# Optimization experiments

Hardware: AMD Instinct MI355X
Metric: run time of the kernel (lower is better)

Reference implementation:

```python
import jax, jax.numpy as jnp
import numpy as np

N = 4096
STD = 0.01


def setup_inputs() -> dict:
    key = jax.random.key(0)
    ks = jax.random.split(key, 16)
    p = lambda k, shape: STD * jax.random.normal(k, shape, dtype=jnp.float32)
    return {
        "t": 0,
        "x": jax.random.normal(ks[0], (N, 1), dtype=jnp.float32),
        "A": jax.random.normal(ks[1], (N, N), dtype=jnp.float32),
        # MLP_A: 2 -> 16 -> 16 -> 1 (ReLU between hidden layers), torch (out,in) layout
        "WA0": p(ks[2], (16, 2)), "bA0": p(ks[3], (16,)),
        "WA1": p(ks[4], (16, 16)), "bA1": p(ks[5], (16,)),
        "WA2": p(ks[6], (1, 16)), "bA2": p(ks[7], (1,)),
        # MLP: 1 -> 16 -> 1 (ReLU after first layer)
        "Wm0": p(ks[8], (16, 1)), "bm0": p(ks[9], (16,)),
        "Wm1": p(ks[10], (1, 16)), "bm1": p(ks[11], (1,)),
        # linear_A: 2 -> 1, no bias; linear_f: 1 -> 1, no bias
        "wA": p(ks[12], (1, 2)),
        "wf": p(ks[13], (1, 1)),
    }


def reference(t, x, A, WA0, bA0, WA1, bA1, WA2, bA2, Wm0, bm0, Wm1, bm1, wA, wf):
    n = x.shape[0]
    # node MLP branch: hidden_list[0] == 1 != 0
    x_N = jax.nn.relu(x @ Wm0.T + bm0) @ Wm1.T + bm1 + x @ wf.T  # (n, 1)
    # all-pairs features: x_a[i, j] = (x_i, x_j)
    x1 = jnp.broadcast_to(x, (n, n))       # row i = x_i repeated
    x2 = jnp.broadcast_to(x.T, (n, n))     # row i = full x vector
    x_a = jnp.stack((x1, x2), axis=-1)     # (n, n, 2)
    # edge MLP (2 -> 16 -> 16 -> 1) + skip linear_A (2 -> 1)
    h = jax.nn.relu(x_a @ WA0.T + bA0)     # (n, n, 16)
    h = jax.nn.relu(h @ WA1.T + bA1)       # (n, n, 16)
    x_e = (h @ WA2.T + bA2)[..., 0]        # (n, n)
    x_12 = (x_a @ wA.T)[..., 0]            # (n, n)
    # adjacency-weighted reduction over neighbors (dim=1)
    x_A = jnp.sum(A * (x_e + x_12), axis=1, keepdims=True)  # (n, 1)
    return x_N + x_A
```

## Files before the change

### kernel.cpp

```cpp
#include <hip/hip_runtime.h>
#include <hip/hip_bf16.h>


#define NN 4096

typedef __fp16 half8  __attribute__((ext_vector_type(8)));
typedef __fp16 half2v __attribute__((ext_vector_type(2)));
typedef __attribute__((ext_vector_type(4)))  float f32x4;
typedef __attribute__((ext_vector_type(16))) float f32x16;

__device__ __forceinline__ half2v cvt2(float lo, float hi) {
    return __builtin_amdgcn_cvt_pkrtz(lo, hi);
}

__global__ __launch_bounds__(256, 4) void odef_kernel(
    const float* __restrict__ x,  const float* __restrict__ A,
    const float* __restrict__ WA0, const float* __restrict__ bA0,
    const float* __restrict__ WA1, const float* __restrict__ bA1,
    const float* __restrict__ WA2, const float* __restrict__ bA2,
    const float* __restrict__ Wm0, const float* __restrict__ bm0,
    const float* __restrict__ Wm1, const float* __restrict__ bm1,
    const float* __restrict__ wA,  const float* __restrict__ wf,
    float* __restrict__ out)
{
    __shared__ float xs[NN];

    const int tid  = threadIdx.x;
    const int wave = tid >> 6;
    const int lane = tid & 63;
    const int n    = lane & 31;
    const int half = lane >> 5;
    const int row  = blockIdx.x * 4 + wave;

    {
        const f32x4* xsrc = (const f32x4*)x;
        f32x4* xdst = (f32x4*)xs;
        #pragma unroll
        for (int i = 0; i < 4; ++i)
            xdst[tid + 256 * i] = xsrc[tid + 256 * i];
    }
    const float xi = x[row];

    union { half2v h2[4]; half8 h8; } au;
    #pragma unroll
    for (int p = 0; p < 4; ++p) {
        float lo = 0.f, hi = 0.f;
        if (n < 16) {
            int k = half * 8 + p * 2;
            lo = WA1[n * 16 + k];
            hi = WA1[n * 16 + k + 1];
        }
        au.h2[p] = cvt2(lo, hi);
    }

    half2v u2h[4], w2h[4];
    #pragma unroll
    for (int p = 0; p < 4; ++p) {
        int k0 = half * 8 + p * 2;
        u2h[p] = cvt2(fmaf(WA0[2 * k0],     xi, bA0[k0]),
                      fmaf(WA0[2 * k0 + 2], xi, bA0[k0 + 1]));
        w2h[p] = cvt2(WA0[2 * k0 + 1], WA0[2 * k0 + 3]);
    }

    half2v wa2h[4], bb[4];
    #pragma unroll
    for (int p = 0; p < 4; ++p) {
        int r  = 2 * p;
        int m0 = (r & 3) + 8 * (r >> 2) + 4 * half;
        wa2h[p] = cvt2(WA2[m0], WA2[m0 + 1]);
        bb[p]   = cvt2(bA1[m0], bA1[m0 + 1]);
    }

    const float wA1h = half ? 0.f : wA[1];
    const float c0h  = half ? 0.f : (bA2[0] + wA[0] * xi);
    const half2v z2 = { (__fp16)0.f, (__fp16)0.f };
    const f32x16 zc = {};

    float acc0 = 0.f, acc1 = 0.f;

    auto body = [&](const f32x4 xv, const f32x4 av) {
        #pragma unroll
        for (int q = 0; q < 4; q += 2) {
            half2v xg0 = cvt2(xv[q], xv[q]);
            union { half2v h2[4]; half8 h8; } b0;
            #pragma unroll
            for (int p = 0; p < 4; ++p)
                b0.h2[p] = __builtin_elementwise_max(w2h[p] * xg0 + u2h[p], z2);
            f32x16 d0 = __builtin_amdgcn_mfma_f32_32x32x16_f16(au.h8, b0.h8, zc, 0, 0, 0);

            half2v xg1 = cvt2(xv[q + 1], xv[q + 1]);
            union { half2v h2[4]; half8 h8; } b1;
            #pragma unroll
            for (int p = 0; p < 4; ++p)
                b1.h2[p] = __builtin_elementwise_max(w2h[p] * xg1 + u2h[p], z2);
            f32x16 d1 = __builtin_amdgcn_mfma_f32_32x32x16_f16(au.h8, b1.h8, zc, 0, 0, 0);

            {
                float pp = fmaf(wA1h, xv[q], c0h);
                #pragma unroll
                for (int p = 0; p < 4; ++p) {
                    half2v t = __builtin_elementwise_max(
                        cvt2(d0[2 * p], d0[2 * p + 1]) + bb[p], z2);
                    pp = __builtin_amdgcn_fdot2(t, wa2h[p], pp, false);
                }
                acc0 = fmaf(av[q], pp, acc0);
            }
            {
                float pp = fmaf(wA1h, xv[q + 1], c0h);
                #pragma unroll
                for (int p = 0; p < 4; ++p) {
                    half2v t = __builtin_elementwise_max(
                        cvt2(d1[2 * p], d1[2 * p + 1]) + bb[p], z2);
                    pp = __builtin_amdgcn_fdot2(t, wa2h[p], pp, false);
                }
                acc1 = fmaf(av[q + 1], pp, acc1);
            }
        }
    };

    __syncthreads();

    const float* ap = A + (size_t)row * NN + 4 * n;
    const f32x4* xls = (const f32x4*)xs;

#define LOADA(dst, p) \
    asm volatile("global_load_dwordx4 %0, %1, off" : "=v"(dst) : "v"(p))
#define WAITV(N) do {                                              \
    asm volatile("s_waitcnt vmcnt(" #N ")" ::: "memory");          \
    __builtin_amdgcn_sched_barrier(0); } while (0)

    __builtin_amdgcn_sched_barrier(0);
    asm volatile("s_waitcnt vmcnt(0)" ::: "memory");
    __builtin_amdgcn_sched_barrier(0);

    f32x4 L0,  L1,  L2,  L3,  L4,  L5,  L6,  L7,
          L8,  L9,  L10, L11, L12, L13, L14, L15,
          L16, L17, L18, L19, L20, L21, L22, L23,
          L24, L25, L26, L27, L28, L29, L30, L31;

    LOADA(L0, ap + 128 * 0);  LOADA(L1, ap + 128 * 1);
    LOADA(L2, ap + 128 * 2);  LOADA(L3, ap + 128 * 3);
    LOADA(L4, ap + 128 * 4);  LOADA(L5, ap + 128 * 5);
    LOADA(L6, ap + 128 * 6);  LOADA(L7, ap + 128 * 7);

#define STEPM(T, CUR, NXT) {                                       \
        f32x4 xv = xls[n + 32 * (T)];                              \
        WAITV(7);                                                  \
        body(xv, CUR);                                             \
        LOADA(NXT, ap + 128 * ((T) + 8)); }

    STEPM(0,  L0,  L8)   STEPM(1,  L1,  L9)   STEPM(2,  L2,  L10)
    STEPM(3,  L3,  L11)  STEPM(4,  L4,  L12)  STEPM(5,  L5,  L13)
    STEPM(6,  L6,  L14)  STEPM(7,  L7,  L15)  STEPM(8,  L8,  L16)
    STEPM(9,  L9,  L17)  STEPM(10, L10, L18)  STEPM(11, L11, L19)
    STEPM(12, L12, L20)  STEPM(13, L13, L21)  STEPM(14, L14, L22)
    STEPM(15, L15, L23)  STEPM(16, L16, L24)  STEPM(17, L17, L25)
    STEPM(18, L18, L26)  STEPM(19, L19, L27)  STEPM(20, L20, L28)
    STEPM(21, L21, L29)  STEPM(22, L22, L30)  STEPM(23, L23, L31)

#define STEPT(T, WN, CUR) {                                        \
        f32x4 xv = xls[n + 32 * (T)];                              \
        WAITV(WN);                                                 \
        body(xv, CUR); }

    STEPT(24, 7, L24) STEPT(25, 6, L25) STEPT(26, 5, L26) STEPT(27, 4, L27)
    STEPT(28, 3, L28) STEPT(29, 2, L29) STEPT(30, 1, L30) STEPT(31, 0, L31)

#undef STEPM
#undef STEPT
#undef LOADA
#undef WAITV

    float acc = acc0 + acc1;
    #pragma unroll
    for (int off = 32; off > 0; off >>= 1)
        acc += __shfl_xor(acc, off);

    if (lane == 0) {
        float xn = fmaf(wf[0], xi, bm1[0]);
        #pragma unroll
        for (int h = 0; h < 16; ++h)
            xn = fmaf(Wm1[h], fmaxf(fmaf(Wm0[h], xi, bm0[h]), 0.f), xn);
        out[row] = xn + acc;
    }
}

extern "C" void kernel_launch(void* const* d_in, const int* in_sizes, int n_in,
                              void* d_out, int out_size, void* d_ws, size_t ws_size,
                              hipStream_t stream) {
    const float* x   = (const float*)d_in[1];
    const float* A   = (const float*)d_in[2];
    const float* WA0 = (const float*)d_in[3];
    const float* bA0 = (const float*)d_in[4];
    const float* WA1 = (const float*)d_in[5];
    const float* bA1 = (const float*)d_in[6];
    const float* WA2 = (const float*)d_in[7];
    const float* bA2 = (const float*)d_in[8];
    const float* Wm0 = (const float*)d_in[9];
    const float* bm0 = (const float*)d_in[10];
    const float* Wm1 = (const float*)d_in[11];
    const float* bm1 = (const float*)d_in[12];
    const float* wA  = (const float*)d_in[13];
    const float* wf  = (const float*)d_in[14];
    float* out = (float*)d_out;

    odef_kernel<<<NN / 4, 256, 0, stream>>>(x, A, WA0, bA0, WA1, bA1, WA2, bA2,
                                            Wm0, bm0, Wm1, bm1, wA, wf, out);
}
```

Before: 145.3 us.

## Pre-convert A to interleaved fp16 in workspace before the main reduction kernel

Adds a conversion kernel that casts A from fp32 to fp16 into the workspace, in an interleaved layout so that each 16-byte load brings eight A values for a lane. The main kernel then streams half the bytes for A and converts them back to fp32 before the same MFMA edge-MLP body. The conversion kernel runs on every call, so it adds a full fp32 read plus an fp16 write of A on top of the main kernel's fp16 read. It also lowers the precision of A. The old fp32 kernel is kept as a fallback when the workspace is too small.

```diff
diff --git a/kernel.cpp b/kernel.cpp
--- a/kernel.cpp
+++ b/kernel.cpp
@@ -13,8 +13,30 @@
     return __builtin_amdgcn_cvt_pkrtz(lo, hi);
 }
 
-__global__ __launch_bounds__(256, 4) void odef_kernel(
-    const float* __restrict__ x,  const float* __restrict__ A,
+__global__ __launch_bounds__(256, 8) void conv_kernel(
+    const float* __restrict__ A, __fp16* __restrict__ B)
+{
+    const int nitems = NN * NN / 8;
+    const int stride = gridDim.x * blockDim.x;
+    for (int i = blockIdx.x * blockDim.x + threadIdx.x; i < nitems; i += stride) {
+        const int row = i >> 9;
+        const int rem = i & 511;
+        const int P = rem >> 5;
+        const int n = rem & 31;
+        const float* s = A + (size_t)row * NN + P * 256 + n * 4;
+        f32x4 lo = *(const f32x4*)s;
+        f32x4 hi = *(const f32x4*)(s + 128);
+        half8 h;
+        h[0] = (__fp16)lo[0]; h[1] = (__fp16)lo[1];
+        h[2] = (__fp16)lo[2]; h[3] = (__fp16)lo[3];
+        h[4] = (__fp16)hi[0]; h[5] = (__fp16)hi[1];
+        h[6] = (__fp16)hi[2]; h[7] = (__fp16)hi[3];
+        *(half8*)(B + (size_t)i * 8) = h;
+    }
+}
+
+__global__ __launch_bounds__(256, 4) void odef_f16(
+    const __fp16* __restrict__ A16, const float* __restrict__ x,
     const float* __restrict__ WA0, const float* __restrict__ bA0,
     const float* __restrict__ WA1, const float* __restrict__ bA1,
     const float* __restrict__ WA2, const float* __restrict__ bA2,
@@ -120,6 +142,182 @@
 
     __syncthreads();
 
+    const __fp16* ap = A16 + (size_t)row * NN + 8 * n;
+    const f32x4* xls = (const f32x4*)xs;
+
+#define LOADA(dst, p) \
+    asm volatile("global_load_dwordx4 %0, %1, off" : "=v"(dst) : "v"(p))
+#define WAITV(N) do {                                              \
+    asm volatile("s_waitcnt vmcnt(" #N ")" ::: "memory");          \
+    __builtin_amdgcn_sched_barrier(0); } while (0)
+
+    __builtin_amdgcn_sched_barrier(0);
+    asm volatile("s_waitcnt vmcnt(0)" ::: "memory");
+    __builtin_amdgcn_sched_barrier(0);
+
+    half8 L0, L1, L2,  L3,  L4,  L5,  L6,  L7,
+          L8, L9, L10, L11, L12, L13, L14, L15;
+
+    LOADA(L0, ap + 256 * 0);  LOADA(L1, ap + 256 * 1);
+    LOADA(L2, ap + 256 * 2);  LOADA(L3, ap + 256 * 3);
+    LOADA(L4, ap + 256 * 4);  LOADA(L5, ap + 256 * 5);
+    LOADA(L6, ap + 256 * 6);  LOADA(L7, ap + 256 * 7);
+
+#define STEPM(T, CUR, NXT) {                                       \
+        f32x4 xa = xls[n + 64 * (T)];                              \
+        f32x4 xb = xls[n + 64 * (T) + 32];                         \
+        WAITV(7);                                                  \
+        f32x4 avA = { (float)CUR[0], (float)CUR[1],                \
+                      (float)CUR[2], (float)CUR[3] };              \
+        f32x4 avB = { (float)CUR[4], (float)CUR[5],                \
+                      (float)CUR[6], (float)CUR[7] };              \
+        body(xa, avA);                                             \
+        body(xb, avB);                                             \
+        LOADA(NXT, ap + 256 * ((T) + 8)); }
+
+    STEPM(0, L0, L8)  STEPM(1, L1, L9)  STEPM(2, L2, L10) STEPM(3, L3, L11)
+    STEPM(4, L4, L12) STEPM(5, L5, L13) STEPM(6, L6, L14) STEPM(7, L7, L15)
+
+#define STEPT(T, WN, CUR) {                                        \
+        f32x4 xa = xls[n + 64 * (T)];                              \
+        f32x4 xb = xls[n + 64 * (T) + 32];                         \
+        WAITV(WN);                                                 \
+        f32x4 avA = { (float)CUR[0], (float)CUR[1],                \
+                      (float)CUR[2], (float)CUR[3] };              \
+        f32x4 avB = { (float)CUR[4], (float)CUR[5],                \
+                      (float)CUR[6], (float)CUR[7] };              \
+        body(xa, avA);                                             \
+        body(xb, avB); }
+
+    STEPT(8,  7, L8)  STEPT(9,  6, L9)  STEPT(10, 5, L10) STEPT(11, 4, L11)
+    STEPT(12, 3, L12) STEPT(13, 2, L13) STEPT(14, 1, L14) STEPT(15, 0, L15)
+
+#undef STEPM
+#undef STEPT
+#undef LOADA
+#undef WAITV
+
+    float acc = acc0 + acc1;
+    #pragma unroll
+    for (int off = 32; off > 0; off >>= 1)
+        acc += __shfl_xor(acc, off);
+
+    if (lane == 0) {
+        float xn = fmaf(wf[0], xi, bm1[0]);
+        #pragma unroll
+        for (int h = 0; h < 16; ++h)
+            xn = fmaf(Wm1[h], fmaxf(fmaf(Wm0[h], xi, bm0[h]), 0.f), xn);
+        out[row] = xn + acc;
+    }
+}
+
+__global__ __launch_bounds__(256, 4) void odef_f32(
+    const float* __restrict__ x,  const float* __restrict__ A,
+    const float* __restrict__ WA0, const float* __restrict__ bA0,
+    const float* __restrict__ WA1, const float* __restrict__ bA1,
+    const float* __restrict__ WA2, const float* __restrict__ bA2,
+    const float* __restrict__ Wm0, const float* __restrict__ bm0,
+    const float* __restrict__ Wm1, const float* __restrict__ bm1,
+    const float* __restrict__ wA,  const float* __restrict__ wf,
+    float* __restrict__ out)
+{
+    __shared__ float xs[NN];
+
+    const int tid  = threadIdx.x;
+    const int wave = tid >> 6;
+    const int lane = tid & 63;
+    const int n    = lane & 31;
+    const int half = lane >> 5;
+    const int row  = blockIdx.x * 4 + wave;
+
+    {
+        const f32x4* xsrc = (const f32x4*)x;
+        f32x4* xdst = (f32x4*)xs;
+        #pragma unroll
+        for (int i = 0; i < 4; ++i)
+            xdst[tid + 256 * i] = xsrc[tid + 256 * i];
+    }
+    const float xi = x[row];
+
+    union { half2v h2[4]; half8 h8; } au;
+    #pragma unroll
+    for (int p = 0; p < 4; ++p) {
+        float lo = 0.f, hi = 0.f;
+        if (n < 16) {
+            int k = half * 8 + p * 2;
+            lo = WA1[n * 16 + k];
+            hi = WA1[n * 16 + k + 1];
+        }
+        au.h2[p] = cvt2(lo, hi);
+    }
+
+    half2v u2h[4], w2h[4];
+    #pragma unroll
+    for (int p = 0; p < 4; ++p) {
+        int k0 = half * 8 + p * 2;
+        u2h[p] = cvt2(fmaf(WA0[2 * k0],     xi, bA0[k0]),
+                      fmaf(WA0[2 * k0 + 2], xi, bA0[k0 + 1]));
+        w2h[p] = cvt2(WA0[2 * k0 + 1], WA0[2 * k0 + 3]);
+    }
+
+    half2v wa2h[4], bb[4];
+    #pragma unroll
+    for (int p = 0; p < 4; ++p) {
+        int r  = 2 * p;
+        int m0 = (r & 3) + 8 * (r >> 2) + 4 * half;
+        wa2h[p] = cvt2(WA2[m0], WA2[m0 + 1]);
+        bb[p]   = cvt2(bA1[m0], bA1[m0 + 1]);
+    }
+
+    const float wA1h = half ? 0.f : wA[1];
+    const float c0h  = half ? 0.f : (bA2[0] + wA[0] * xi);
+    const half2v z2 = { (__fp16)0.f, (__fp16)0.f };
+    const f32x16 zc = {};
+
+    float acc0 = 0.f, acc1 = 0.f;
+
+    auto body = [&](const f32x4 xv, const f32x4 av) {
+        #pragma unroll
+        for (int q = 0; q < 4; q += 2) {
+            half2v xg0 = cvt2(xv[q], xv[q]);
+            union { half2v h2[4]; half8 h8; } b0;
+            #pragma unroll
+            for (int p = 0; p < 4; ++p)
+                b0.h2[p] = __builtin_elementwise_max(w2h[p] * xg0 + u2h[p], z2);
+            f32x16 d0 = __builtin_amdgcn_mfma_f32_32x32x16_f16(au.h8, b0.h8, zc, 0, 0, 0);
+
+            half2v xg1 = cvt2(xv[q + 1], xv[q + 1]);
+            union { half2v h2[4]; half8 h8; } b1;
+            #pragma unroll
+            for (int p = 0; p < 4; ++p)
+                b1.h2[p] = __builtin_elementwise_max(w2h[p] * xg1 + u2h[p], z2);
+            f32x16 d1 = __builtin_amdgcn_mfma_f32_32x32x16_f16(au.h8, b1.h8, zc, 0, 0, 0);
+
+            {
+                float pp = fmaf(wA1h, xv[q], c0h);
+                #pragma unroll
+                for (int p = 0; p < 4; ++p) {
+                    half2v t = __builtin_elementwise_max(
+                        cvt2(d0[2 * p], d0[2 * p + 1]) + bb[p], z2);
+                    pp = __builtin_amdgcn_fdot2(t, wa2h[p], pp, false);
+                }
+                acc0 = fmaf(av[q], pp, acc0);
+            }
+            {
+                float pp = fmaf(wA1h, xv[q + 1], c0h);
+                #pragma unroll
+                for (int p = 0; p < 4; ++p) {
+                    half2v t = __builtin_elementwise_max(
+                        cvt2(d1[2 * p], d1[2 * p + 1]) + bb[p], z2);
+                    pp = __builtin_amdgcn_fdot2(t, wa2h[p], pp, false);
+                }
+                acc1 = fmaf(av[q + 1], pp, acc1);
+            }
+        }
+    };
+
+    __syncthreads();
+
     const float* ap = A + (size_t)row * NN + 4 * n;
     const f32x4* xls = (const f32x4*)xs;
 
@@ -204,6 +402,15 @@
     const float* wf  = (const float*)d_in[14];
     float* out = (float*)d_out;
 
-    odef_kernel<<<NN / 4, 256, 0, stream>>>(x, A, WA0, bA0, WA1, bA1, WA2, bA2,
-                                            Wm0, bm0, Wm1, bm1, wA, wf, out);
+    if (ws_size >= (size_t)NN * NN * 2) {
+        __fp16* A16 = (__fp16*)d_ws;
+        conv_kernel<<<2048, 256, 0, stream>>>(A, A16);
+        odef_f16<<<NN / 4, 256, 0, stream>>>(A16, x, WA0, bA0, WA1, bA1,
+                                             WA2, bA2, Wm0, bm0, Wm1, bm1,
+                                             wA, wf, out);
+    } else {
+        odef_f32<<<NN / 4, 256, 0, stream>>>(x, A, WA0, bA0, WA1, bA1,
+                                             WA2, bA2, Wm0, bm0, Wm1, bm1,
+                                             wA, wf, out);
+    }
 }
```

Result: slower. 164.5 us (+13.2%).
